# Kernel tuning notes

Measured on AMD Instinct MI355X. Metric: run time of the kernel, lower is better.

## Reference

```python
import jax, jax.numpy as jnp
import numpy as np

N_NODES = 100000
N_EDGES = 1600000
N_GRAPHS = 512


def gcn_conv(x, src, dst, W, b, num_nodes):
    """PyG GCNConv: add self-loops, sym-normalize, aggregate, add bias."""
    xw = x @ W  # [N, out]
    # degree over destination nodes, +1 for the implicit self-loop
    deg = jax.ops.segment_sum(jnp.ones(src.shape[0], xw.dtype), dst,
                              num_segments=num_nodes) + 1.0
    dinv = jax.lax.rsqrt(deg)  # deg >= 1, safe
    norm = dinv[src] * dinv[dst]  # [E]
    agg = jax.ops.segment_sum(xw[src] * norm[:, None], dst,
                              num_segments=num_nodes)
    # self-loop contribution: dinv[i]^2 * xw[i]
    agg = agg + xw * (dinv * dinv)[:, None]
    return agg + b


def global_mean_pool(x, batch, num_graphs):
    sums = jax.ops.segment_sum(x, batch, num_segments=num_graphs)
    cnts = jax.ops.segment_sum(jnp.ones(x.shape[0], x.dtype), batch,
                               num_segments=num_graphs)
    return sums / jnp.maximum(cnts, 1.0)[:, None]


def setup_inputs() -> dict:
    key = jax.random.key(0)
    ks = jax.random.split(key, 9)
    x = jax.random.normal(ks[0], (N_NODES, 3), dtype=jnp.float32)
    edge_index = jax.random.randint(ks[1], (2, N_EDGES), 0, N_NODES, dtype=jnp.int64)
    batch = jnp.sort(jax.random.randint(ks[2], (N_NODES,), 0, N_GRAPHS, dtype=jnp.int64))
    W1 = jax.random.normal(ks[3], (3, 32), dtype=jnp.float32) * 0.5
    b1 = jax.random.normal(ks[4], (32,), dtype=jnp.float32) * 0.1
    W2 = jax.random.normal(ks[5], (32, 32), dtype=jnp.float32) * 0.2
    b2 = jax.random.normal(ks[6], (32,), dtype=jnp.float32) * 0.1
    Wl = jax.random.normal(ks[7], (32, 2), dtype=jnp.float32) * 0.2
    bl = jax.random.normal(ks[8], (2,), dtype=jnp.float32) * 0.1
    return {"x": x, "edge_index": edge_index, "batch": batch,
            "W1": W1, "b1": b1, "W2": W2, "b2": b2, "Wl": Wl, "bl": bl}


def reference(x, edge_index, batch, W1, b1, W2, b2, Wl, bl):
    src, dst = edge_index[0], edge_index[1]
    h = jax.nn.relu(gcn_conv(x, src, dst, W1, b1, N_NODES))
    h = jax.nn.relu(gcn_conv(h, src, dst, W2, b2, N_NODES))
    g = global_mean_pool(h, batch, N_GRAPHS)  # [G, 32]
    return g @ Wl + bl  # [G, 2]
```

## Files before the change

### kernel.cpp

```cpp
#include <hip/hip_runtime.h>
#include <hip/hip_fp16.h>

#define NN 100000
#define NE 1600000
#define NG 512
#define F  32

#define BSH    8
#define BNODES 256
#define NB     ((NN + BNODES - 1) / BNODES)
#define CAP    5120
#define PCHUNK 4096
#define EPT    8
#define NWGP   ((NE + PCHUNK - 1) / PCHUNK)

__global__ void k_partition(const int* __restrict__ src, const int* __restrict__ dst,
                            int* __restrict__ cursor, int* __restrict__ part) {
    __shared__ int   s_cnt[NB];
    __shared__ int   s_scan[512];
    __shared__ int   s_lstart[NB];
    __shared__ int   s_base[NB];
    __shared__ int   lsort[PCHUNK];
    __shared__ short lbkt[PCHUNK];
    int tid = threadIdx.x;
    for (int i = tid; i < NB; i += 512) s_cnt[i] = 0;
    __syncthreads();
    int e0 = blockIdx.x * PCHUNK;
    int e1 = min(e0 + PCHUNK, NE);
    int pk[EPT]; short bk[EPT];
    int m = 0;
#pragma unroll
    for (int k = 0; k < EPT; ++k) {
        int e = e0 + tid + k * 512;
        if (e < e1) {
            int d = dst[e];
            pk[m] = (src[e] << 8) | (d & (BNODES - 1));
            bk[m] = (short)(d >> BSH);
            atomicAdd(&s_cnt[bk[m]], 1);
            ++m;
        }
    }
    __syncthreads();
    int cv = (tid < NB) ? s_cnt[tid] : 0;
    s_scan[tid] = cv;
    __syncthreads();
    for (int o = 1; o < 512; o <<= 1) {
        int t = (tid >= o) ? s_scan[tid - o] : 0;
        __syncthreads();
        s_scan[tid] += t;
        __syncthreads();
    }
    if (tid < NB) {
        s_lstart[tid] = s_scan[tid] - cv;
        if (cv) s_base[tid] = tid * CAP + atomicAdd(&cursor[tid], cv);
        s_cnt[tid] = 0;
    }
    __syncthreads();
    for (int k = 0; k < m; ++k) {
        int b = bk[k];
        int r = s_lstart[b] + atomicAdd(&s_cnt[b], 1);
        lsort[r] = pk[k];
        lbkt[r]  = (short)b;
    }
    __syncthreads();
    int cnt = e1 - e0;
    for (int i = tid; i < cnt; i += 512) {
        int b = lbkt[i];
        part[s_base[b] + (i - s_lstart[b])] = lsort[i];
    }
}

__global__ void k_fill2a(const int* __restrict__ part, const int* __restrict__ cursor,
                         const float* __restrict__ x,
                         int* __restrict__ rowpack, float* __restrict__ dinv,
                         float4* __restrict__ xd) {
    __shared__ int cnt[BNODES];
    __shared__ int lds[BNODES];
    int b = blockIdx.x, tid = threadIdx.x;
    int node0 = b << BSH;
    int s0 = b * CAP, s1 = s0 + cursor[b];
    cnt[tid] = 0;
    __syncthreads();
    for (int i = s0 + tid; i < s1; i += 256) atomicAdd(&cnt[part[i] & (BNODES - 1)], 1);
    __syncthreads();
    int c = cnt[tid];
    lds[tid] = c;
    __syncthreads();
    for (int o = 1; o < 256; o <<= 1) {
        int t = (tid >= o) ? lds[tid - o] : 0;
        __syncthreads();
        lds[tid] += t;
        __syncthreads();
    }
    int excl = lds[tid] - c;
    int n = node0 + tid;
    if (n < NN) {
        rowpack[n] = ((s0 + excl) << 10) | c;
        float d = rsqrtf((float)c + 1.0f);
        dinv[n] = d;
        xd[n] = make_float4(d * x[n * 3 + 0], d * x[n * 3 + 1], d * x[n * 3 + 2], d);
    }
}

__global__ void k_fill2b(const int* __restrict__ part, const int* __restrict__ cursor,
                         const int* __restrict__ rowpack, const float4* __restrict__ xd,
                         const float* __restrict__ W1, const float* __restrict__ b1,
                         int* __restrict__ csr, __half2* __restrict__ g1) {
    __shared__ int lcsr[CAP];
    __shared__ int off[BNODES];
    __shared__ float W1s[3 * F];
    __shared__ float b1s[F];
    int b = blockIdx.x, tid = threadIdx.x;
    int node0 = b << BSH;
    int s0 = b * CAP;
    int cnt = cursor[b];
    if (tid < 3 * F) W1s[tid] = W1[tid];
    if (tid < F) b1s[tid] = b1[tid];
    int n = node0 + tid;
    int pack = (n < NN) ? rowpack[n] : (s0 << 10);
    off[tid] = (pack >> 10) - s0;
    __syncthreads();
    for (int i = tid; i < cnt; i += 256) {
        int p = part[s0 + i];
        int pos = atomicAdd(&off[p & (BNODES - 1)], 1);
        lcsr[pos] = p >> 8;
    }
    __syncthreads();
    for (int i = tid; i < cnt; i += 256) csr[s0 + i] = lcsr[i];
    if (n < NN) {
        int deg = pack & 1023;
        int beg = (pack >> 10) - s0;
        int end = beg + deg;
        float ax = 0.0f, ay = 0.0f, az = 0.0f;
        int e = beg;
        for (; e + 3 < end; e += 4) {
            int i0 = lcsr[e], i1 = lcsr[e + 1], i2 = lcsr[e + 2], i3 = lcsr[e + 3];
            float4 v0 = xd[i0], v1 = xd[i1], v2 = xd[i2], v3 = xd[i3];
            ax += (v0.x + v1.x) + (v2.x + v3.x);
            ay += (v0.y + v1.y) + (v2.y + v3.y);
            az += (v0.z + v1.z) + (v2.z + v3.z);
        }
        for (; e < end; ++e) {
            float4 v = xd[lcsr[e]];
            ax += v.x; ay += v.y; az += v.z;
        }
        float4 sf = xd[n];
        float dn = sf.w;
        float cx = dn * (ax + sf.x), cy = dn * (ay + sf.y), cz = dn * (az + sf.z);
        __half2 tmp[16];
#pragma unroll
        for (int j = 0; j < 16; ++j) {
            int f0 = 2 * j, f1 = 2 * j + 1;
            float v0 = cx * W1s[f0] + cy * W1s[F + f0] + cz * W1s[2 * F + f0] + b1s[f0];
            float v1 = cx * W1s[f1] + cy * W1s[F + f1] + cz * W1s[2 * F + f1] + b1s[f1];
            tmp[j] = __floats2half2_rn(dn * fmaxf(v0, 0.0f), dn * fmaxf(v1, 0.0f));
        }
        uint4* hv = (uint4*)(g1 + (size_t)n * 16);
        const uint4* tv = (const uint4*)tmp;
        hv[0] = tv[0]; hv[1] = tv[1]; hv[2] = tv[2]; hv[3] = tv[3];
    }
}

__global__ void k_gather2p(const int* __restrict__ rowpack, const int* __restrict__ csr,
                           const __half2* __restrict__ g1, const float* __restrict__ dinv,
                           const int* __restrict__ batch,
                           const float* __restrict__ W2, const float* __restrict__ b2,
                           float* __restrict__ gsum) {
    __shared__ float W2s[F * F];
    __shared__ float b2s[F];
    __shared__ float ts[16][F];
    __shared__ float hs[16][F];
    __shared__ int bat[16];
    int tid = threadIdx.x;
    int nb = blockIdx.x * 16;
    for (int i = tid; i < F * F; i += 256) W2s[i] = W2[i];
    if (tid < F) b2s[tid] = b2[tid];
    if (tid < 16) bat[tid] = batch[nb + tid];
    int nl = tid >> 4, j = tid & 15;
    int n = nb + nl;
    {
        int pack = rowpack[n];
        int beg = pack >> 10, end = beg + (pack & 1023);
        float ax = 0.0f, ay = 0.0f;
        int e = beg;
        for (; e + 3 < end; e += 4) {
            int s0 = csr[e], s1 = csr[e + 1], s2 = csr[e + 2], s3 = csr[e + 3];
            float2 v0 = __half22float2(g1[s0 * 16 + j]);
            float2 v1 = __half22float2(g1[s1 * 16 + j]);
            float2 v2 = __half22float2(g1[s2 * 16 + j]);
            float2 v3 = __half22float2(g1[s3 * 16 + j]);
            ax += (v0.x + v1.x) + (v2.x + v3.x);
            ay += (v0.y + v1.y) + (v2.y + v3.y);
        }
        for (; e < end; ++e) {
            float2 v = __half22float2(g1[csr[e] * 16 + j]);
            ax += v.x; ay += v.y;
        }
        float dn = dinv[n];
        float2 sf = __half22float2(g1[n * 16 + j]);
        ts[nl][2 * j]     = dn * (ax + sf.x);
        ts[nl][2 * j + 1] = dn * (ay + sf.y);
    }
    __syncthreads();
    {
        int f = tid & 31;
        int nn0 = tid >> 5;
#pragma unroll
        for (int pass = 0; pass < 2; ++pass) {
            int nn = nn0 + pass * 8;
            float acc = b2s[f];
#pragma unroll
            for (int k = 0; k < F; ++k) acc += ts[nn][k] * W2s[k * F + f];
            hs[nn][f] = fmaxf(acc, 0.0f);
        }
    }
    __syncthreads();
    if (tid < F) {
        int g0 = bat[0], gmax = bat[15];
        for (int g = g0; g <= gmax; ++g) {
            float s = 0.0f;
#pragma unroll
            for (int i = 0; i < 16; ++i) if (bat[i] == g) s += hs[i][tid];
            atomicAdd(&gsum[g * F + tid], s);
        }
    }
}

__global__ void k_head(const float* __restrict__ gsum, const int* __restrict__ batch,
                       const float* __restrict__ Wl, const float* __restrict__ bl,
                       float* __restrict__ out) {
    int g = blockIdx.x * blockDim.x + threadIdx.x;
    if (g >= NG) return;
    int lo = 0, hi = NN;
    while (lo < hi) { int m = (lo + hi) >> 1; if (batch[m] < g) lo = m + 1; else hi = m; }
    int s = lo;
    lo = 0; hi = NN;
    while (lo < hi) { int m = (lo + hi) >> 1; if (batch[m] < g + 1) lo = m + 1; else hi = m; }
    float inv = 1.0f / fmaxf((float)(lo - s), 1.0f);
    float a0 = 0.0f, a1 = 0.0f;
#pragma unroll
    for (int k = 0; k < F; ++k) {
        float m = gsum[g * F + k] * inv;
        a0 += m * Wl[k * 2 + 0];
        a1 += m * Wl[k * 2 + 1];
    }
    out[g * 2 + 0] = a0 + bl[0];
    out[g * 2 + 1] = a1 + bl[1];
}

extern "C" void kernel_launch(void* const* d_in, const int* in_sizes, int n_in,
                              void* d_out, int out_size, void* d_ws, size_t ws_size,
                              hipStream_t stream) {
    const float* x     = (const float*)d_in[0];
    const int*   eidx  = (const int*)d_in[1];
    const int*   batch = (const int*)d_in[2];
    const float* W1    = (const float*)d_in[3];
    const float* b1    = (const float*)d_in[4];
    const float* W2    = (const float*)d_in[5];
    const float* b2    = (const float*)d_in[6];
    const float* Wl    = (const float*)d_in[7];
    const float* bl    = (const float*)d_in[8];
    float*       out   = (float*)d_out;

    const int* src = eidx;
    const int* dst = eidx + NE;

    char* base = (char*)d_ws;
    size_t off = 0;
    auto alloc = [&](size_t bytes) {
        void* p = base + off;
        off = (off + bytes + 127) & ~(size_t)127;
        return p;
    };
    int*     cursor  = (int*)alloc(NB * sizeof(int) + (size_t)NG * F * sizeof(float));
    float*   gsum    = (float*)(cursor + NB);
    int*     rowpack = (int*)alloc(NN * sizeof(int));
    int*     part    = (int*)alloc((size_t)NB * CAP * sizeof(int));
    int*     csr     = (int*)alloc((size_t)NB * CAP * sizeof(int));
    float*   dinv    = (float*)alloc(NN * sizeof(float));
    float4*  xd      = (float4*)alloc(NN * sizeof(float4));
    __half2* g1      = (__half2*)alloc((size_t)NN * 16 * sizeof(__half2));

    const int B = 256;
    const int gG16 = NN / 16;

    hipMemsetAsync(cursor, 0, NB * sizeof(int) + (size_t)NG * F * sizeof(float), stream);

    k_partition<<<NWGP, 512, 0, stream>>>(src, dst, cursor, part);
    k_fill2a   <<<NB,   B,   0, stream>>>(part, cursor, x, rowpack, dinv, xd);
    k_fill2b   <<<NB,   B,   0, stream>>>(part, cursor, rowpack, xd, W1, b1, csr, g1);

    k_gather2p<<<gG16, B, 0, stream>>>(rowpack, csr, g1, dinv, batch, W2, b2, gsum);

    k_head<<<(NG + B - 1) / B, B, 0, stream>>>(gsum, batch, Wl, bl, out);
}
```

Before: 170.9 us.

## Use wave-shuffle scans, unroll gathers by 8, fuse head into last block

The LDS Hillis-Steele scans in partition and fill2a become wavefront shuffle scans plus a small per-wave sum combine, which removes many block barriers. The gather loops in fill2b and gather2p are unrolled to eight neighbours so more loads are in flight. The separate head kernel is dropped: a last-block-done atomic counter lets the final gather2p block compute the pooled mean and linear head, saving one launch. In exchange there is an extra atomic and threadfence per block, and the tail work runs serially on one block.

```diff
diff --git a/kernel.cpp b/kernel.cpp
--- a/kernel.cpp
+++ b/kernel.cpp
@@ -17,9 +17,9 @@
 __global__ void k_partition(const int* __restrict__ src, const int* __restrict__ dst,
                             int* __restrict__ cursor, int* __restrict__ part) {
     __shared__ int   s_cnt[NB];
-    __shared__ int   s_scan[512];
     __shared__ int   s_lstart[NB];
     __shared__ int   s_base[NB];
+    __shared__ int   wsum[8];
     __shared__ int   lsort[PCHUNK];
     __shared__ short lbkt[PCHUNK];
     int tid = threadIdx.x;
@@ -42,16 +42,19 @@
     }
     __syncthreads();
     int cv = (tid < NB) ? s_cnt[tid] : 0;
-    s_scan[tid] = cv;
-    __syncthreads();
-    for (int o = 1; o < 512; o <<= 1) {
-        int t = (tid >= o) ? s_scan[tid - o] : 0;
-        __syncthreads();
-        s_scan[tid] += t;
-        __syncthreads();
-    }
+    int v = cv;
+#pragma unroll
+    for (int o = 1; o < 64; o <<= 1) {
+        int t = __shfl_up(v, o, 64);
+        if ((tid & 63) >= o) v += t;
+    }
+    if ((tid & 63) == 63) wsum[tid >> 6] = v;
+    __syncthreads();
+    int add = 0;
+    for (int w = 0; w < (tid >> 6); ++w) add += wsum[w];
+    int excl = v + add - cv;
     if (tid < NB) {
-        s_lstart[tid] = s_scan[tid] - cv;
+        s_lstart[tid] = excl;
         if (cv) s_base[tid] = tid * CAP + atomicAdd(&cursor[tid], cv);
         s_cnt[tid] = 0;
     }
@@ -75,7 +78,7 @@
                          int* __restrict__ rowpack, float* __restrict__ dinv,
                          float4* __restrict__ xd) {
     __shared__ int cnt[BNODES];
-    __shared__ int lds[BNODES];
+    __shared__ int wsum[4];
     int b = blockIdx.x, tid = threadIdx.x;
     int node0 = b << BSH;
     int s0 = b * CAP, s1 = s0 + cursor[b];
@@ -84,15 +87,17 @@
     for (int i = s0 + tid; i < s1; i += 256) atomicAdd(&cnt[part[i] & (BNODES - 1)], 1);
     __syncthreads();
     int c = cnt[tid];
-    lds[tid] = c;
-    __syncthreads();
-    for (int o = 1; o < 256; o <<= 1) {
-        int t = (tid >= o) ? lds[tid - o] : 0;
-        __syncthreads();
-        lds[tid] += t;
-        __syncthreads();
-    }
-    int excl = lds[tid] - c;
+    int v = c;
+#pragma unroll
+    for (int o = 1; o < 64; o <<= 1) {
+        int t = __shfl_up(v, o, 64);
+        if ((tid & 63) >= o) v += t;
+    }
+    if ((tid & 63) == 63) wsum[tid >> 6] = v;
+    __syncthreads();
+    int add = 0;
+    for (int w = 0; w < (tid >> 6); ++w) add += wsum[w];
+    int excl = v + add - c;
     int n = node0 + tid;
     if (n < NN) {
         rowpack[n] = ((s0 + excl) << 10) | c;
@@ -133,12 +138,12 @@
         int end = beg + deg;
         float ax = 0.0f, ay = 0.0f, az = 0.0f;
         int e = beg;
-        for (; e + 3 < end; e += 4) {
-            int i0 = lcsr[e], i1 = lcsr[e + 1], i2 = lcsr[e + 2], i3 = lcsr[e + 3];
-            float4 v0 = xd[i0], v1 = xd[i1], v2 = xd[i2], v3 = xd[i3];
-            ax += (v0.x + v1.x) + (v2.x + v3.x);
-            ay += (v0.y + v1.y) + (v2.y + v3.y);
-            az += (v0.z + v1.z) + (v2.z + v3.z);
+        for (; e + 7 < end; e += 8) {
+#pragma unroll
+            for (int u = 0; u < 8; ++u) {
+                float4 v = xd[lcsr[e + u]];
+                ax += v.x; ay += v.y; az += v.z;
+            }
         }
         for (; e < end; ++e) {
             float4 v = xd[lcsr[e]];
@@ -165,12 +170,15 @@
                            const __half2* __restrict__ g1, const float* __restrict__ dinv,
                            const int* __restrict__ batch,
                            const float* __restrict__ W2, const float* __restrict__ b2,
-                           float* __restrict__ gsum) {
+                           const float* __restrict__ Wl, const float* __restrict__ bl,
+                           float* __restrict__ gsum, int* __restrict__ done,
+                           float* __restrict__ out) {
     __shared__ float W2s[F * F];
     __shared__ float b2s[F];
     __shared__ float ts[16][F];
     __shared__ float hs[16][F];
     __shared__ int bat[16];
+    __shared__ int slast;
     int tid = threadIdx.x;
     int nb = blockIdx.x * 16;
     for (int i = tid; i < F * F; i += 256) W2s[i] = W2[i];
@@ -183,6 +191,20 @@
         int beg = pack >> 10, end = beg + (pack & 1023);
         float ax = 0.0f, ay = 0.0f;
         int e = beg;
+        for (; e + 7 < end; e += 8) {
+            int s0 = csr[e],     s1 = csr[e + 1], s2 = csr[e + 2], s3 = csr[e + 3];
+            int s4 = csr[e + 4], s5 = csr[e + 5], s6 = csr[e + 6], s7 = csr[e + 7];
+            float2 v0 = __half22float2(g1[s0 * 16 + j]);
+            float2 v1 = __half22float2(g1[s1 * 16 + j]);
+            float2 v2 = __half22float2(g1[s2 * 16 + j]);
+            float2 v3 = __half22float2(g1[s3 * 16 + j]);
+            float2 v4 = __half22float2(g1[s4 * 16 + j]);
+            float2 v5 = __half22float2(g1[s5 * 16 + j]);
+            float2 v6 = __half22float2(g1[s6 * 16 + j]);
+            float2 v7 = __half22float2(g1[s7 * 16 + j]);
+            ax += ((v0.x + v1.x) + (v2.x + v3.x)) + ((v4.x + v5.x) + (v6.x + v7.x));
+            ay += ((v0.y + v1.y) + (v2.y + v3.y)) + ((v4.y + v5.y) + (v6.y + v7.y));
+        }
         for (; e + 3 < end; e += 4) {
             int s0 = csr[e], s1 = csr[e + 1], s2 = csr[e + 2], s3 = csr[e + 3];
             float2 v0 = __half22float2(g1[s0 * 16 + j]);
@@ -224,28 +246,32 @@
             atomicAdd(&gsum[g * F + tid], s);
         }
     }
-}
-
-__global__ void k_head(const float* __restrict__ gsum, const int* __restrict__ batch,
-                       const float* __restrict__ Wl, const float* __restrict__ bl,
-                       float* __restrict__ out) {
-    int g = blockIdx.x * blockDim.x + threadIdx.x;
-    if (g >= NG) return;
-    int lo = 0, hi = NN;
-    while (lo < hi) { int m = (lo + hi) >> 1; if (batch[m] < g) lo = m + 1; else hi = m; }
-    int s = lo;
-    lo = 0; hi = NN;
-    while (lo < hi) { int m = (lo + hi) >> 1; if (batch[m] < g + 1) lo = m + 1; else hi = m; }
-    float inv = 1.0f / fmaxf((float)(lo - s), 1.0f);
-    float a0 = 0.0f, a1 = 0.0f;
-#pragma unroll
-    for (int k = 0; k < F; ++k) {
-        float m = gsum[g * F + k] * inv;
-        a0 += m * Wl[k * 2 + 0];
-        a1 += m * Wl[k * 2 + 1];
-    }
-    out[g * 2 + 0] = a0 + bl[0];
-    out[g * 2 + 1] = a1 + bl[1];
+    __syncthreads();
+    if (tid == 0) {
+        __threadfence();
+        slast = (atomicAdd(done, 1) == (int)gridDim.x - 1) ? 1 : 0;
+    }
+    __syncthreads();
+    if (slast) {
+        __threadfence();
+        for (int g = tid; g < NG; g += 256) {
+            int lo = 0, hi = NN;
+            while (lo < hi) { int m = (lo + hi) >> 1; if (batch[m] < g) lo = m + 1; else hi = m; }
+            int s = lo;
+            lo = 0; hi = NN;
+            while (lo < hi) { int m = (lo + hi) >> 1; if (batch[m] < g + 1) lo = m + 1; else hi = m; }
+            float inv = 1.0f / fmaxf((float)(lo - s), 1.0f);
+            float a0 = 0.0f, a1 = 0.0f;
+#pragma unroll
+            for (int k = 0; k < F; ++k) {
+                float mn = gsum[g * F + k] * inv;
+                a0 += mn * Wl[k * 2 + 0];
+                a1 += mn * Wl[k * 2 + 1];
+            }
+            out[g * 2 + 0] = a0 + bl[0];
+            out[g * 2 + 1] = a1 + bl[1];
+        }
+    }
 }
 
 extern "C" void kernel_launch(void* const* d_in, const int* in_sizes, int n_in,
@@ -272,8 +298,9 @@
         off = (off + bytes + 127) & ~(size_t)127;
         return p;
     };
-    int*     cursor  = (int*)alloc(NB * sizeof(int) + (size_t)NG * F * sizeof(float));
-    float*   gsum    = (float*)(cursor + NB);
+    int*     cursor  = (int*)alloc((NB + 1) * sizeof(int) + (size_t)NG * F * sizeof(float));
+    int*     done    = cursor + NB;
+    float*   gsum    = (float*)(done + 1);
     int*     rowpack = (int*)alloc(NN * sizeof(int));
     int*     part    = (int*)alloc((size_t)NB * CAP * sizeof(int));
     int*     csr     = (int*)alloc((size_t)NB * CAP * sizeof(int));
@@ -284,13 +311,12 @@
     const int B = 256;
     const int gG16 = NN / 16;
 
-    hipMemsetAsync(cursor, 0, NB * sizeof(int) + (size_t)NG * F * sizeof(float), stream);
+    hipMemsetAsync(cursor, 0, (NB + 1) * sizeof(int) + (size_t)NG * F * sizeof(float), stream);
 
     k_partition<<<NWGP, 512, 0, stream>>>(src, dst, cursor, part);
     k_fill2a   <<<NB,   B,   0, stream>>>(part, cursor, x, rowpack, dinv, xd);
     k_fill2b   <<<NB,   B,   0, stream>>>(part, cursor, rowpack, xd, W1, b1, csr, g1);
 
-    k_gather2p<<<gG16, B, 0, stream>>>(rowpack, csr, g1, dinv, batch, W2, b2, gsum);
-
-    k_head<<<(NG + B - 1) / B, B, 0, stream>>>(gsum, batch, Wl, bl, out);
-}
+    k_gather2p<<<gG16, B, 0, stream>>>(rowpack, csr, g1, dinv, batch, W2, b2,
+                                       Wl, bl, gsum, done, out);
+}
```

After: 281.3 us. 64.6% more time.
